# Kernel optimization log

Measured on AMD Instinct MI355X. Metric: run time of the kernel, lower is better.

The kernel has to match this reference:

```python
import jax, jax.numpy as jnp
import numpy as np

B, S, D, H = 4, 2048, 1024, 16
HD = D // H  # head dim = 64


def setup_inputs() -> dict:
    key = jax.random.key(0)
    ks = jax.random.split(key, 6)
    scale = D ** -0.5
    x = jax.random.normal(ks[0], (B, S, D), dtype=jnp.float32)
    # per-head q/k/v projections stacked: [H, D, HD] (bias-free, as in GPT Head)
    Wq = jax.random.normal(ks[1], (H, D, HD), dtype=jnp.float32) * scale
    Wk = jax.random.normal(ks[2], (H, D, HD), dtype=jnp.float32) * scale
    Wv = jax.random.normal(ks[3], (H, D, HD), dtype=jnp.float32) * scale
    # output projection Linear(D, D) with bias
    Wp = jax.random.normal(ks[4], (D, D), dtype=jnp.float32) * scale
    bp = jax.random.normal(ks[5], (D,), dtype=jnp.float32) * 0.01
    return {"x": x, "Wq": Wq, "Wk": Wk, "Wv": Wv, "Wp": Wp, "bp": bp}


def reference(x, Wq, Wk, Wv, Wp, bp):
    # q,k,v: [B, H, S, HD]
    q = jnp.einsum("bsd,hdk->bhsk", x, Wq)
    k = jnp.einsum("bsd,hdk->bhsk", x, Wk)
    v = jnp.einsum("bsd,hdk->bhsk", x, Wv)
    scale = HD ** -0.5
    # attention scores [B, H, S, S] with causal mask
    scores = jnp.einsum("bhsk,bhtk->bhst", q, k) * scale
    causal = jnp.tril(jnp.ones((S, S), dtype=bool))
    scores = jnp.where(causal, scores, jnp.finfo(scores.dtype).min)
    att = jax.nn.softmax(scores, axis=-1)
    out = jnp.einsum("bhst,bhtk->bhsk", att, v)  # [B, H, S, HD]
    # concat heads -> [B, S, D], then output projection
    out = out.transpose(0, 2, 1, 3).reshape(B, S, D)
    return out @ Wp + bp
```

## Files before the change

kernel.cpp:

```cpp
#include <hip/hip_runtime.h>
#include <stdint.h>

#define B_  4
#define S_  2048
#define D_  1024
#define H_  16
#define HD_ 64

typedef __attribute__((ext_vector_type(8))) short bf16x8;
typedef __attribute__((ext_vector_type(4))) short bf16x4;
typedef __attribute__((ext_vector_type(4))) float f32x4;

#define MFMA32(a, b, c) __builtin_amdgcn_mfma_f32_16x16x32_bf16(a, b, c, 0, 0, 0)

__device__ __forceinline__ unsigned short f2bf(float f) {
  union { float f; uint32_t u; } cv; cv.f = f;
  uint32_t x = cv.u;
  uint32_t r = (x + 0x7fffu + ((x >> 16) & 1u)) >> 16;
  return (unsigned short)r;
}

__device__ __forceinline__ unsigned short f2bf_rz(float f) {
  union { float f; uint32_t u; } cv; cv.f = f;
  return (unsigned short)(cv.u >> 16);
}

__device__ __forceinline__ void gload_lds16(const unsigned short* g, unsigned short* l) {
  __builtin_amdgcn_global_load_lds((const __attribute__((address_space(1))) void*)g,
                                   (__attribute__((address_space(3))) void*)l, 16, 0, 0);
}

__global__ void k_cast_x(const float* __restrict__ x, unsigned short* __restrict__ xb) {
  size_t i = ((size_t)blockIdx.x * 256 + threadIdx.x) * 8;
  float4 a = *(const float4*)(x + i);
  float4 b = *(const float4*)(x + i + 4);
  bf16x8 o;
  o[0] = (short)f2bf(a.x); o[1] = (short)f2bf(a.y);
  o[2] = (short)f2bf(a.z); o[3] = (short)f2bf(a.w);
  o[4] = (short)f2bf(b.x); o[5] = (short)f2bf(b.y);
  o[6] = (short)f2bf(b.z); o[7] = (short)f2bf(b.w);
  *(bf16x8*)(xb + i) = o;
}

__global__ void k_wqkv_t(const float* __restrict__ Wq, const float* __restrict__ Wk,
                         const float* __restrict__ Wv, unsigned short* __restrict__ W1T) {
  __shared__ unsigned short tile[64][65];
  const float* W = (blockIdx.z == 0) ? Wq : (blockIdx.z == 1) ? Wk : Wv;
  int h = blockIdx.y;
  int d0 = blockIdx.x * 64;
  int tx = threadIdx.x & 63;
  int tg = threadIdx.x >> 6;
  const float* src = W + (size_t)h * (D_ * HD_) + (size_t)d0 * HD_;
#pragma unroll
  for (int r = 0; r < 16; ++r) {
    int dy = tg * 16 + r;
    tile[tx][dy] = f2bf(src[(size_t)dy * HD_ + tx]);
  }
  __syncthreads();
  unsigned short* dst = W1T + ((size_t)blockIdx.z * 1024 + (size_t)h * 64) * 1024 + d0;
#pragma unroll
  for (int r = 0; r < 16; ++r) {
    int hd = tg * 16 + r;
    dst[(size_t)hd * 1024 + tx] = tile[hd][tx];
  }
}

__global__ void k_wp_t(const float* __restrict__ Wp, unsigned short* __restrict__ WpT) {
  __shared__ unsigned short tile[64][65];
  int n0 = blockIdx.x * 64, k0 = blockIdx.y * 64;
  int tx = threadIdx.x & 63;
  int tg = threadIdx.x >> 6;
#pragma unroll
  for (int r = 0; r < 16; ++r) {
    int ky = tg * 16 + r;
    tile[tx][ky] = f2bf(Wp[(size_t)(k0 + ky) * D_ + n0 + tx]);
  }
  __syncthreads();
#pragma unroll
  for (int r = 0; r < 16; ++r) {
    int ny = tg * 16 + r;
    WpT[(size_t)(n0 + ny) * D_ + k0 + tx] = tile[ny][tx];
  }
}

__device__ __forceinline__ void stage_half(const unsigned short* g0, unsigned short* l0, int tid) {
  int r0 = tid >> 2, s0 = tid & 3;
  gload_lds16(g0 + (size_t)r0 * 1024 + ((s0 ^ ((r0 >> 1) & 3)) << 3), l0 + tid * 8);
  int r1 = r0 + 128;
  gload_lds16(g0 + (size_t)r1 * 1024 + ((s0 ^ ((r1 >> 1) & 3)) << 3), l0 + 4096 + tid * 8);
}

__device__ __forceinline__ bf16x8 rd_swz(const unsigned short* base, int row, int g) {
  return *(const bf16x8*)&base[row * 32 + ((g ^ ((row >> 1) & 3)) << 3)];
}

__global__ __launch_bounds__(512, 2) void k_gemm_qk(const unsigned short* __restrict__ xb,
                                                    const unsigned short* __restrict__ W1T,
                                                    unsigned short* __restrict__ qb,
                                                    unsigned short* __restrict__ kb) {
  __shared__ __align__(16) unsigned short As[32768];
  __shared__ __align__(16) unsigned short Bs[32768];
  int tid = threadIdx.x;
  int lane = tid & 63;
  int wid = tid >> 6;
  int c = lane & 15, g = lane >> 4;
  int wr = wid >> 2, wc = wid & 3;
  int bid = blockIdx.x;
  int xcd = bid & 7, idx = bid >> 3;
  int by = (xcd << 2) | (idx & 3);
  int bx = idx >> 2;
  int m0 = by << 8, n0 = bx << 8;
  const unsigned short* gA = xb + (size_t)m0 * 1024;
  const unsigned short* gB = W1T + (size_t)n0 * 1024;

  f32x4 acc[8][4];
#pragma unroll
  for (int i = 0; i < 8; ++i)
#pragma unroll
    for (int n = 0; n < 4; ++n) acc[i][n] = (f32x4){0.f, 0.f, 0.f, 0.f};

  stage_half(gA + 0,  As + 0, tid);
  stage_half(gB + 0,  Bs + 0, tid);
  stage_half(gA + 32, As + 8192, tid);
  stage_half(gB + 32, Bs + 8192, tid);

  for (int t = 0; t < 16; ++t) {
    int sl = (t & 1) << 14;
    int so = sl ^ 16384;
    int kn = (t + 1) << 6;
    bool pf = (t < 15);
    const unsigned short* Asl = As + sl;
    const unsigned short* Bsl = Bs + sl;
    bf16x8 bf[4];

    asm volatile("s_waitcnt vmcnt(4)" ::: "memory");
    __builtin_amdgcn_s_barrier();
    if (pf) stage_half(gA + kn, As + so, tid);
#pragma unroll
    for (int n = 0; n < 4; ++n) bf[n] = rd_swz(Bsl, wc * 64 + n * 16 + c, g);
    {
      bf16x8 af[4];
#pragma unroll
      for (int j = 0; j < 4; ++j) af[j] = rd_swz(Asl, wr * 128 + j * 16 + c, g);
      __builtin_amdgcn_s_setprio(1);
#pragma unroll
      for (int j = 0; j < 4; ++j)
#pragma unroll
        for (int n = 0; n < 4; ++n) acc[j][n] = MFMA32(af[j], bf[n], acc[j][n]);
      __builtin_amdgcn_s_setprio(0);
    }
    if (pf) stage_half(gB + kn, Bs + so, tid);
    {
      bf16x8 af[4];
#pragma unroll
      for (int j = 0; j < 4; ++j) af[j] = rd_swz(Asl, wr * 128 + (4 + j) * 16 + c, g);
      __builtin_amdgcn_s_setprio(1);
#pragma unroll
      for (int j = 0; j < 4; ++j)
#pragma unroll
        for (int n = 0; n < 4; ++n) acc[4 + j][n] = MFMA32(af[j], bf[n], acc[4 + j][n]);
      __builtin_amdgcn_s_setprio(0);
    }
    asm volatile("s_waitcnt vmcnt(4)" ::: "memory");
    __builtin_amdgcn_s_barrier();
    if (pf) stage_half(gA + kn + 32, As + so + 8192, tid);
#pragma unroll
    for (int n = 0; n < 4; ++n) bf[n] = rd_swz(Bsl + 8192, wc * 64 + n * 16 + c, g);
    {
      bf16x8 af[4];
#pragma unroll
      for (int j = 0; j < 4; ++j) af[j] = rd_swz(Asl + 8192, wr * 128 + j * 16 + c, g);
      __builtin_amdgcn_s_setprio(1);
#pragma unroll
      for (int j = 0; j < 4; ++j)
#pragma unroll
        for (int n = 0; n < 4; ++n) acc[j][n] = MFMA32(af[j], bf[n], acc[j][n]);
      __builtin_amdgcn_s_setprio(0);
    }
    if (pf) stage_half(gB + kn + 32, Bs + so + 8192, tid);
    {
      bf16x8 af[4];
#pragma unroll
      for (int j = 0; j < 4; ++j) af[j] = rd_swz(Asl + 8192, wr * 128 + (4 + j) * 16 + c, g);
      __builtin_amdgcn_s_setprio(1);
#pragma unroll
      for (int j = 0; j < 4; ++j)
#pragma unroll
        for (int n = 0; n < 4; ++n) acc[4 + j][n] = MFMA32(af[j], bf[n], acc[4 + j][n]);
      __builtin_amdgcn_s_setprio(0);
    }
  }

  int Cnb = n0 + wc * 64;
  int qkv = Cnb >> 10;
  int h = (Cnb >> 6) & 15;
  int b = m0 >> 11;
  int s0 = m0 & 2047;
  unsigned short* dst = ((qkv == 0) ? qb : kb) + ((size_t)(b * 16 + h) * S_) * HD_;
  float sc = (qkv == 0) ? 0.125f : 1.0f;
#pragma unroll
  for (int mrep = 0; mrep < 8; ++mrep)
#pragma unroll
    for (int n = 0; n < 4; ++n)
#pragma unroll
      for (int r = 0; r < 4; ++r) {
        int s = s0 + wr * 128 + mrep * 16 + 4 * g + r;
        int hd = n * 16 + c;
        dst[(size_t)s * HD_ + hd] = f2bf(acc[mrep][n][r] * sc);
      }
}

__global__ __launch_bounds__(256) void k_gemm_vt(const unsigned short* __restrict__ W1T,
                                                 const unsigned short* __restrict__ xb,
                                                 unsigned short* __restrict__ vt) {
  __shared__ __align__(16) unsigned short As[128 * 32];
  __shared__ __align__(16) unsigned short Bs[128 * 32];
  const int K = 1024;
  int tid = threadIdx.x;
  int lane = tid & 63;
  int w = tid >> 6;
  int c = lane & 15, g = lane >> 4;
  int wr = w >> 1, wc = w & 1;
  int nwg = gridDim.x * gridDim.y;
  int bid = blockIdx.y * gridDim.x + blockIdx.x;
  int swzb = (bid & 7) * (nwg >> 3) + (bid >> 3);
  int bx = swzb % gridDim.x, by = swzb / gridDim.x;
  int m0 = by * 128;
  int n0 = bx * 128;
  const unsigned short* Av = W1T + (size_t)2048 * 1024;
  f32x4 acc[4][4];
#pragma unroll
  for (int m = 0; m < 4; ++m)
#pragma unroll
    for (int n = 0; n < 4; ++n) acc[m][n] = (f32x4){0.f, 0.f, 0.f, 0.f};

  int t0 = tid, t1 = tid + 256;
  const unsigned short* ga0 = Av + (size_t)(m0 + (t0 >> 2)) * K + 8 * (t0 & 3);
  const unsigned short* ga1 = Av + (size_t)(m0 + (t1 >> 2)) * K + 8 * (t1 & 3);
  const unsigned short* gb0 = xb + (size_t)(n0 + (t0 >> 2)) * K + 8 * (t0 & 3);
  const unsigned short* gb1 = xb + (size_t)(n0 + (t1 >> 2)) * K + 8 * (t1 & 3);

  for (int kk = 0; kk < K; kk += 32) {
    __syncthreads();
    gload_lds16(ga0 + kk, &As[t0 * 8]);
    gload_lds16(ga1 + kk, &As[t1 * 8]);
    gload_lds16(gb0 + kk, &Bs[t0 * 8]);
    gload_lds16(gb1 + kk, &Bs[t1 * 8]);
    __syncthreads();
    bf16x8 af[4], bfr[4];
#pragma unroll
    for (int m = 0; m < 4; ++m)
      af[m] = *(const bf16x8*)&As[(wr * 64 + m * 16 + c) * 32 + 8 * g];
#pragma unroll
    for (int n = 0; n < 4; ++n)
      bfr[n] = *(const bf16x8*)&Bs[(wc * 64 + n * 16 + c) * 32 + 8 * g];
#pragma unroll
    for (int m = 0; m < 4; ++m)
#pragma unroll
      for (int n = 0; n < 4; ++n) acc[m][n] = MFMA32(af[m], bfr[n], acc[m][n]);
  }

  int b = (n0 >> 11);
#pragma unroll
  for (int m = 0; m < 4; ++m)
#pragma unroll
    for (int n = 0; n < 4; ++n)
#pragma unroll
      for (int r = 0; r < 4; ++r) {
        int vm = m0 + wr * 64 + m * 16 + 4 * g + r;
        int Cn = n0 + wc * 64 + n * 16 + c;
        int s = Cn & 2047;
        vt[((size_t)(b << 10) + vm) * S_ + s] = f2bf(acc[m][n][r]);
      }
}

__device__ __forceinline__ void stage_kv(const unsigned short* kp, const unsigned short* vp,
                                         int tb, unsigned short* Ks, unsigned short* Vs,
                                         int tid) {
  int i0 = tid, i1 = tid + 256;
  int r0 = i0 >> 3, ch0 = ((i0 & 7) ^ (r0 & 7)) << 3;
  int r1 = i1 >> 3, ch1 = ((i1 & 7) ^ (r1 & 7)) << 3;
  gload_lds16(kp + (size_t)(tb + r0) * HD_ + ch0, &Ks[i0 * 8]);
  gload_lds16(kp + (size_t)(tb + r1) * HD_ + ch1, &Ks[i1 * 8]);
  gload_lds16(vp + (size_t)r0 * S_ + tb + ch0, &Vs[i0 * 8]);
  gload_lds16(vp + (size_t)r1 * S_ + tb + ch1, &Vs[i1 * 8]);
}

__global__ __launch_bounds__(256) void k_attn(const unsigned short* __restrict__ qb,
                                              const unsigned short* __restrict__ kb,
                                              const unsigned short* __restrict__ vt,
                                              unsigned short* __restrict__ attn) {
  __shared__ __align__(16) unsigned short Ks[2][64 * 64];
  __shared__ __align__(16) unsigned short Vs[2][64 * 64];
  int tid = threadIdx.x;
  int lane = tid & 63;
  int w = tid >> 6;
  int c = lane & 15, g = lane >> 4;
  int swz = ((blockIdx.x & 7) << 6) | (blockIdx.x >> 3);
  int bh = swz >> 3;
  int pr = swz & 7;
  const unsigned short* kp = kb + (size_t)bh * S_ * HD_;
  const unsigned short* vp = vt + (size_t)bh * HD_ * S_;
  int b = bh >> 4, h = bh & 15;

  for (int p = 0; p < 2; ++p) {
    int j = p ? (15 - pr) : pr;
    int q0w = j * 128 + w * 32;
    const unsigned short* qp = qb + ((size_t)bh * S_ + q0w) * HD_;
    bf16x8 qf[2][2];
#pragma unroll
    for (int qs = 0; qs < 2; ++qs)
#pragma unroll
      for (int h2 = 0; h2 < 2; ++h2)
        qf[qs][h2] = *(const bf16x8*)(qp + (size_t)(qs * 16 + c) * HD_ + h2 * 32 + 8 * g);

    const f32x4 fz = {0.f, 0.f, 0.f, 0.f};
    f32x4 oacc[4][2];
#pragma unroll
    for (int c4 = 0; c4 < 4; ++c4)
#pragma unroll
      for (int qs = 0; qs < 2; ++qs) oacc[c4][qs] = fz;
    float m[2] = {-1e30f, -1e30f};
    float l[2] = {0.f, 0.f};

    int nkb = 2 * j + 2;
    int nkw = (q0w + 95) >> 6;

    stage_kv(kp, vp, 0, Ks[0], Vs[0], tid);
    __syncthreads();

    for (int kt = 0; kt < nkb; ++kt) {
      int cur = kt & 1;
      if (kt + 1 < nkb) stage_kv(kp, vp, (kt + 1) << 6, Ks[cur ^ 1], Vs[cur ^ 1], tid);
      if (kt < nkw) {
        int tb = kt << 6;
        const unsigned short* KsC = Ks[cur];
        const unsigned short* VsC = Vs[cur];
        f32x4 st[4][2];
#pragma unroll
        for (int k4 = 0; k4 < 4; ++k4) {
          int row = k4 * 16 + c;
          int rx = row & 7;
          bf16x8 a0 = *(const bf16x8*)&KsC[row * 64 + ((g ^ rx) << 3)];
          bf16x8 a1 = *(const bf16x8*)&KsC[row * 64 + (((4 + g) ^ rx) << 3)];
#pragma unroll
          for (int qs = 0; qs < 2; ++qs) {
            f32x4 t0 = MFMA32(a0, qf[qs][0], fz);
            st[k4][qs] = MFMA32(a1, qf[qs][1], t0);
          }
        }
        if (tb + 63 > q0w) {
#pragma unroll
          for (int k4 = 0; k4 < 4; ++k4)
#pragma unroll
            for (int qs = 0; qs < 2; ++qs)
#pragma unroll
              for (int r = 0; r < 4; ++r)
                if (tb + k4 * 16 + 4 * g + r > q0w + qs * 16 + c) st[k4][qs][r] = -1e30f;
        }
        bf16x8 pa[2][2];
#pragma unroll
        for (int qs = 0; qs < 2; ++qs) {
          float mx = -1e30f;
#pragma unroll
          for (int k4 = 0; k4 < 4; ++k4)
#pragma unroll
            for (int r = 0; r < 4; ++r) mx = fmaxf(mx, st[k4][qs][r]);
          mx = fmaxf(mx, __shfl_xor(mx, 16));
          mx = fmaxf(mx, __shfl_xor(mx, 32));
          if (!__all(mx - m[qs] <= 8.f)) {
            float m_new = fmaxf(m[qs], mx);
            float resc = __expf(m[qs] - m_new);
            m[qs] = m_new;
            float rb0 = __shfl(resc, 4 * g + 0);
            float rb1 = __shfl(resc, 4 * g + 1);
            float rb2 = __shfl(resc, 4 * g + 2);
            float rb3 = __shfl(resc, 4 * g + 3);
#pragma unroll
            for (int c4 = 0; c4 < 4; ++c4) {
              oacc[c4][qs][0] *= rb0; oacc[c4][qs][1] *= rb1;
              oacc[c4][qs][2] *= rb2; oacc[c4][qs][3] *= rb3;
            }
            l[qs] *= resc;
          }
          float mh = m[qs];
          float rs = 0.f;
#pragma unroll
          for (int k4 = 0; k4 < 4; ++k4)
#pragma unroll
            for (int r = 0; r < 4; ++r) {
              float e = __expf(st[k4][qs][r] - mh);
              st[k4][qs][r] = e;
              rs += e;
            }
          rs += __shfl_xor(rs, 16);
          rs += __shfl_xor(rs, 32);
          l[qs] += rs;
#pragma unroll
          for (int ks = 0; ks < 2; ++ks)
#pragma unroll
            for (int jj = 0; jj < 8; ++jj)
              pa[qs][ks][jj] = (short)f2bf_rz(st[ks * 2 + (jj >> 2)][qs][jj & 3]);
        }
#pragma unroll
        for (int c4 = 0; c4 < 4; ++c4) {
          int row = c4 * 16 + c;
          int rx = row & 7;
#pragma unroll
          for (int ks = 0; ks < 2; ++ks) {
            int e0 = ks * 32 + 4 * g;
            int e1 = e0 + 16;
            int s0 = (((e0 >> 3) ^ rx) << 3) | (e0 & 7);
            int s1 = (((e1 >> 3) ^ rx) << 3) | (e1 & 7);
            bf16x4 v0 = *(const bf16x4*)&VsC[row * 64 + s0];
            bf16x4 v1 = *(const bf16x4*)&VsC[row * 64 + s1];
            bf16x8 vf;
            vf[0] = v0[0]; vf[1] = v0[1]; vf[2] = v0[2]; vf[3] = v0[3];
            vf[4] = v1[0]; vf[5] = v1[1]; vf[6] = v1[2]; vf[7] = v1[3];
#pragma unroll
            for (int qs = 0; qs < 2; ++qs)
              oacc[c4][qs] = MFMA32(pa[qs][ks], vf, oacc[c4][qs]);
          }
        }
      }
      __syncthreads();
    }
#pragma unroll
    for (int qs = 0; qs < 2; ++qs) {
      float linv = 1.f / l[qs];
      float lb0 = __shfl(linv, 4 * g + 0);
      float lb1 = __shfl(linv, 4 * g + 1);
      float lb2 = __shfl(linv, 4 * g + 2);
      float lb3 = __shfl(linv, 4 * g + 3);
      float lb[4] = {lb0, lb1, lb2, lb3};
      unsigned short* op = attn + ((size_t)b * S_ + q0w + qs * 16) * D_ + h * HD_;
#pragma unroll
      for (int c4 = 0; c4 < 4; ++c4)
#pragma unroll
        for (int r = 0; r < 4; ++r)
          op[(size_t)(4 * g + r) * D_ + c4 * 16 + c] = f2bf(oacc[c4][qs][r] * lb[r]);
    }
  }
}

__global__ __launch_bounds__(256) void k_gemm_out(const unsigned short* __restrict__ at,
                                                  const unsigned short* __restrict__ WpT,
                                                  const float* __restrict__ bp,
                                                  float* __restrict__ out) {
  __shared__ __align__(16) unsigned short As[128 * 32];
  __shared__ __align__(16) unsigned short Bs[128 * 32];
  const int K = 1024;
  int tid = threadIdx.x;
  int lane = tid & 63;
  int w = tid >> 6;
  int c = lane & 15, g = lane >> 4;
  int wr = w >> 1, wc = w & 1;
  int nwg = gridDim.x * gridDim.y;
  int bid = blockIdx.y * gridDim.x + blockIdx.x;
  int swzb = (bid & 7) * (nwg >> 3) + (bid >> 3);
  int bx = swzb % gridDim.x, by = swzb / gridDim.x;
  int m0 = by * 128;
  int n0 = bx * 128;
  f32x4 acc[4][4];
#pragma unroll
  for (int m = 0; m < 4; ++m)
#pragma unroll
    for (int n = 0; n < 4; ++n) acc[m][n] = (f32x4){0.f, 0.f, 0.f, 0.f};

  int t0 = tid, t1 = tid + 256;
  const unsigned short* ga0 = at + (size_t)(m0 + (t0 >> 2)) * K + 8 * (t0 & 3);
  const unsigned short* ga1 = at + (size_t)(m0 + (t1 >> 2)) * K + 8 * (t1 & 3);
  const unsigned short* gb0 = WpT + (size_t)(n0 + (t0 >> 2)) * K + 8 * (t0 & 3);
  const unsigned short* gb1 = WpT + (size_t)(n0 + (t1 >> 2)) * K + 8 * (t1 & 3);

  for (int kk = 0; kk < K; kk += 32) {
    __syncthreads();
    gload_lds16(ga0 + kk, &As[t0 * 8]);
    gload_lds16(ga1 + kk, &As[t1 * 8]);
    gload_lds16(gb0 + kk, &Bs[t0 * 8]);
    gload_lds16(gb1 + kk, &Bs[t1 * 8]);
    __syncthreads();
    bf16x8 af[4], bfr[4];
#pragma unroll
    for (int m = 0; m < 4; ++m)
      af[m] = *(const bf16x8*)&As[(wr * 64 + m * 16 + c) * 32 + 8 * g];
#pragma unroll
    for (int n = 0; n < 4; ++n)
      bfr[n] = *(const bf16x8*)&Bs[(wc * 64 + n * 16 + c) * 32 + 8 * g];
#pragma unroll
    for (int m = 0; m < 4; ++m)
#pragma unroll
      for (int n = 0; n < 4; ++n) acc[m][n] = MFMA32(af[m], bfr[n], acc[m][n]);
  }

#pragma unroll
  for (int m = 0; m < 4; ++m)
#pragma unroll
    for (int n = 0; n < 4; ++n)
#pragma unroll
      for (int r = 0; r < 4; ++r) {
        int R = m0 + wr * 64 + m * 16 + 4 * g + r;
        int Cn = n0 + wc * 64 + n * 16 + c;
        out[(size_t)R * D_ + Cn] = acc[m][n][r] + bp[Cn];
      }
}

extern "C" void kernel_launch(void* const* d_in, const int* in_sizes, int n_in,
                              void* d_out, int out_size, void* d_ws, size_t ws_size,
                              hipStream_t stream) {
  const float* x  = (const float*)d_in[0];
  const float* Wq = (const float*)d_in[1];
  const float* Wk = (const float*)d_in[2];
  const float* Wv = (const float*)d_in[3];
  const float* Wp = (const float*)d_in[4];
  const float* bp = (const float*)d_in[5];
  float* out = (float*)d_out;
  char* ws = (char*)d_ws;
  unsigned short* xb  = (unsigned short*)(ws);
  unsigned short* w1t = (unsigned short*)(ws + (size_t)(16u << 20));
  unsigned short* wpt = (unsigned short*)(ws + (size_t)(22u << 20));
  unsigned short* qb  = (unsigned short*)(ws + (size_t)(24u << 20));
  unsigned short* kb  = (unsigned short*)(ws + (size_t)(40u << 20));
  unsigned short* vt  = (unsigned short*)(ws + (size_t)(56u << 20));
  unsigned short* at  = xb;

  k_cast_x<<<dim3(4096), dim3(256), 0, stream>>>(x, xb);
  k_wqkv_t<<<dim3(16, 16, 3), dim3(256), 0, stream>>>(Wq, Wk, Wv, w1t);
  k_wp_t<<<dim3(16, 16), dim3(256), 0, stream>>>(Wp, wpt);
  k_gemm_qk<<<dim3(256), dim3(512), 0, stream>>>(xb, w1t, qb, kb);
  k_gemm_vt<<<dim3(64, 8), dim3(256), 0, stream>>>(w1t, xb, vt);
  k_attn<<<dim3(512), dim3(256), 0, stream>>>(qb, kb, vt, at);
  k_gemm_out<<<dim3(8, 64), dim3(256), 0, stream>>>(at, wpt, bp, out);
}
```

Before: 184.8 us.

## Halve attention query tile per block, double grid, use exp2 with folded log2e scale

```diff
diff --git a/kernel.cpp b/kernel.cpp
--- a/kernel.cpp
+++ b/kernel.cpp
@@ -23,6 +23,14 @@
 __device__ __forceinline__ unsigned short f2bf_rz(float f) {
   union { float f; uint32_t u; } cv; cv.f = f;
   return (unsigned short)(cv.u >> 16);
+}
+
+__device__ __forceinline__ float fexp2(float x) {
+#if __has_builtin(__builtin_amdgcn_exp2f)
+  return __builtin_amdgcn_exp2f(x);
+#else
+  return exp2f(x);
+#endif
 }
 
 __device__ __forceinline__ void gload_lds16(const unsigned short* g, unsigned short* l) {
@@ -197,7 +205,7 @@
   int b = m0 >> 11;
   int s0 = m0 & 2047;
   unsigned short* dst = ((qkv == 0) ? qb : kb) + ((size_t)(b * 16 + h) * S_) * HD_;
-  float sc = (qkv == 0) ? 0.125f : 1.0f;
+  float sc = (qkv == 0) ? 0.18033688011112042f : 1.0f;
 #pragma unroll
   for (int mrep = 0; mrep < 8; ++mrep)
 #pragma unroll
@@ -296,35 +304,29 @@
   int lane = tid & 63;
   int w = tid >> 6;
   int c = lane & 15, g = lane >> 4;
-  int swz = ((blockIdx.x & 7) << 6) | (blockIdx.x >> 3);
-  int bh = swz >> 3;
-  int pr = swz & 7;
+  int swz = ((blockIdx.x & 7) << 7) | (blockIdx.x >> 3);
+  int bh = swz >> 4;
+  int pr = swz & 15;
   const unsigned short* kp = kb + (size_t)bh * S_ * HD_;
   const unsigned short* vp = vt + (size_t)bh * HD_ * S_;
   int b = bh >> 4, h = bh & 15;
 
   for (int p = 0; p < 2; ++p) {
-    int j = p ? (15 - pr) : pr;
-    int q0w = j * 128 + w * 32;
+    int j = p ? (31 - pr) : pr;
+    int q0w = j * 64 + w * 16;
     const unsigned short* qp = qb + ((size_t)bh * S_ + q0w) * HD_;
-    bf16x8 qf[2][2];
-#pragma unroll
-    for (int qs = 0; qs < 2; ++qs)
-#pragma unroll
-      for (int h2 = 0; h2 < 2; ++h2)
-        qf[qs][h2] = *(const bf16x8*)(qp + (size_t)(qs * 16 + c) * HD_ + h2 * 32 + 8 * g);
+    bf16x8 qf[2];
+#pragma unroll
+    for (int h2 = 0; h2 < 2; ++h2)
+      qf[h2] = *(const bf16x8*)(qp + (size_t)c * HD_ + h2 * 32 + 8 * g);
 
     const f32x4 fz = {0.f, 0.f, 0.f, 0.f};
-    f32x4 oacc[4][2];
-#pragma unroll
-    for (int c4 = 0; c4 < 4; ++c4)
-#pragma unroll
-      for (int qs = 0; qs < 2; ++qs) oacc[c4][qs] = fz;
-    float m[2] = {-1e30f, -1e30f};
-    float l[2] = {0.f, 0.f};
-
-    int nkb = 2 * j + 2;
-    int nkw = (q0w + 95) >> 6;
+    f32x4 oacc[4];
+#pragma unroll
+    for (int c4 = 0; c4 < 4; ++c4) oacc[c4] = fz;
+    float m = -1e30f, l = 0.f;
+
+    int nkb = j + 1;
 
     stage_kv(kp, vp, 0, Ks[0], Vs[0], tid);
     __syncthreads();
@@ -332,76 +334,67 @@
     for (int kt = 0; kt < nkb; ++kt) {
       int cur = kt & 1;
       if (kt + 1 < nkb) stage_kv(kp, vp, (kt + 1) << 6, Ks[cur ^ 1], Vs[cur ^ 1], tid);
-      if (kt < nkw) {
+      {
         int tb = kt << 6;
         const unsigned short* KsC = Ks[cur];
         const unsigned short* VsC = Vs[cur];
-        f32x4 st[4][2];
+        f32x4 st[4];
 #pragma unroll
         for (int k4 = 0; k4 < 4; ++k4) {
           int row = k4 * 16 + c;
           int rx = row & 7;
           bf16x8 a0 = *(const bf16x8*)&KsC[row * 64 + ((g ^ rx) << 3)];
           bf16x8 a1 = *(const bf16x8*)&KsC[row * 64 + (((4 + g) ^ rx) << 3)];
-#pragma unroll
-          for (int qs = 0; qs < 2; ++qs) {
-            f32x4 t0 = MFMA32(a0, qf[qs][0], fz);
-            st[k4][qs] = MFMA32(a1, qf[qs][1], t0);
-          }
+          f32x4 t0 = MFMA32(a0, qf[0], fz);
+          st[k4] = MFMA32(a1, qf[1], t0);
         }
         if (tb + 63 > q0w) {
 #pragma unroll
           for (int k4 = 0; k4 < 4; ++k4)
 #pragma unroll
-            for (int qs = 0; qs < 2; ++qs)
-#pragma unroll
-              for (int r = 0; r < 4; ++r)
-                if (tb + k4 * 16 + 4 * g + r > q0w + qs * 16 + c) st[k4][qs][r] = -1e30f;
+            for (int r = 0; r < 4; ++r)
+              if (tb + k4 * 16 + 4 * g + r > q0w + c) st[k4][r] = -1e30f;
         }
-        bf16x8 pa[2][2];
-#pragma unroll
-        for (int qs = 0; qs < 2; ++qs) {
-          float mx = -1e30f;
-#pragma unroll
-          for (int k4 = 0; k4 < 4; ++k4)
-#pragma unroll
-            for (int r = 0; r < 4; ++r) mx = fmaxf(mx, st[k4][qs][r]);
-          mx = fmaxf(mx, __shfl_xor(mx, 16));
-          mx = fmaxf(mx, __shfl_xor(mx, 32));
-          if (!__all(mx - m[qs] <= 8.f)) {
-            float m_new = fmaxf(m[qs], mx);
-            float resc = __expf(m[qs] - m_new);
-            m[qs] = m_new;
-            float rb0 = __shfl(resc, 4 * g + 0);
-            float rb1 = __shfl(resc, 4 * g + 1);
-            float rb2 = __shfl(resc, 4 * g + 2);
-            float rb3 = __shfl(resc, 4 * g + 3);
-#pragma unroll
-            for (int c4 = 0; c4 < 4; ++c4) {
-              oacc[c4][qs][0] *= rb0; oacc[c4][qs][1] *= rb1;
-              oacc[c4][qs][2] *= rb2; oacc[c4][qs][3] *= rb3;
-            }
-            l[qs] *= resc;
+        float mx = -1e30f;
+#pragma unroll
+        for (int k4 = 0; k4 < 4; ++k4)
+#pragma unroll
+          for (int r = 0; r < 4; ++r) mx = fmaxf(mx, st[k4][r]);
+        mx = fmaxf(mx, __shfl_xor(mx, 16));
+        mx = fmaxf(mx, __shfl_xor(mx, 32));
+        if (!__all(mx - m <= 8.f)) {
+          float m_new = fmaxf(m, mx);
+          float resc = fexp2(m - m_new);
+          m = m_new;
+          float rb0 = __shfl(resc, 4 * g + 0);
+          float rb1 = __shfl(resc, 4 * g + 1);
+          float rb2 = __shfl(resc, 4 * g + 2);
+          float rb3 = __shfl(resc, 4 * g + 3);
+#pragma unroll
+          for (int c4 = 0; c4 < 4; ++c4) {
+            oacc[c4][0] *= rb0; oacc[c4][1] *= rb1;
+            oacc[c4][2] *= rb2; oacc[c4][3] *= rb3;
           }
-          float mh = m[qs];
-          float rs = 0.f;
-#pragma unroll
-          for (int k4 = 0; k4 < 4; ++k4)
-#pragma unroll
-            for (int r = 0; r < 4; ++r) {
-              float e = __expf(st[k4][qs][r] - mh);
-              st[k4][qs][r] = e;
-              rs += e;
-            }
-          rs += __shfl_xor(rs, 16);
-          rs += __shfl_xor(rs, 32);
-          l[qs] += rs;
-#pragma unroll
-          for (int ks = 0; ks < 2; ++ks)
-#pragma unroll
-            for (int jj = 0; jj < 8; ++jj)
-              pa[qs][ks][jj] = (short)f2bf_rz(st[ks * 2 + (jj >> 2)][qs][jj & 3]);
+          l *= resc;
         }
+        float rs = 0.f;
+#pragma unroll
+        for (int k4 = 0; k4 < 4; ++k4)
+#pragma unroll
+          for (int r = 0; r < 4; ++r) {
+            float e = fexp2(st[k4][r] - m);
+            st[k4][r] = e;
+            rs += e;
+          }
+        rs += __shfl_xor(rs, 16);
+        rs += __shfl_xor(rs, 32);
+        l += rs;
+        bf16x8 pa[2];
+#pragma unroll
+        for (int ks = 0; ks < 2; ++ks)
+#pragma unroll
+          for (int jj = 0; jj < 8; ++jj)
+            pa[ks][jj] = (short)f2bf_rz(st[ks * 2 + (jj >> 2)][jj & 3]);
 #pragma unroll
         for (int c4 = 0; c4 < 4; ++c4) {
           int row = c4 * 16 + c;
@@ -417,29 +410,24 @@
             bf16x8 vf;
             vf[0] = v0[0]; vf[1] = v0[1]; vf[2] = v0[2]; vf[3] = v0[3];
             vf[4] = v1[0]; vf[5] = v1[1]; vf[6] = v1[2]; vf[7] = v1[3];
-#pragma unroll
-            for (int qs = 0; qs < 2; ++qs)
-              oacc[c4][qs] = MFMA32(pa[qs][ks], vf, oacc[c4][qs]);
+            oacc[c4] = MFMA32(pa[ks], vf, oacc[c4]);
           }
         }
       }
       __syncthreads();
     }
-#pragma unroll
-    for (int qs = 0; qs < 2; ++qs) {
-      float linv = 1.f / l[qs];
-      float lb0 = __shfl(linv, 4 * g + 0);
-      float lb1 = __shfl(linv, 4 * g + 1);
-      float lb2 = __shfl(linv, 4 * g + 2);
-      float lb3 = __shfl(linv, 4 * g + 3);
-      float lb[4] = {lb0, lb1, lb2, lb3};
-      unsigned short* op = attn + ((size_t)b * S_ + q0w + qs * 16) * D_ + h * HD_;
-#pragma unroll
-      for (int c4 = 0; c4 < 4; ++c4)
-#pragma unroll
-        for (int r = 0; r < 4; ++r)
-          op[(size_t)(4 * g + r) * D_ + c4 * 16 + c] = f2bf(oacc[c4][qs][r] * lb[r]);
-    }
+    float linv = 1.f / l;
+    float lb0 = __shfl(linv, 4 * g + 0);
+    float lb1 = __shfl(linv, 4 * g + 1);
+    float lb2 = __shfl(linv, 4 * g + 2);
+    float lb3 = __shfl(linv, 4 * g + 3);
+    float lb[4] = {lb0, lb1, lb2, lb3};
+    unsigned short* op = attn + ((size_t)b * S_ + q0w) * D_ + h * HD_;
+#pragma unroll
+    for (int c4 = 0; c4 < 4; ++c4)
+#pragma unroll
+      for (int r = 0; r < 4; ++r)
+        op[(size_t)(4 * g + r) * D_ + c4 * 16 + c] = f2bf(oacc[c4][r] * lb[r]);
   }
 }
 
@@ -529,6 +517,6 @@
   k_wp_t<<<dim3(16, 16), dim3(256), 0, stream>>>(Wp, wpt);
   k_gemm_qk<<<dim3(256), dim3(512), 0, stream>>>(xb, w1t, qb, kb);
   k_gemm_vt<<<dim3(64, 8), dim3(256), 0, stream>>>(w1t, xb, vt);
-  k_attn<<<dim3(512), dim3(256), 0, stream>>>(qb, kb, vt, at);
+  k_attn<<<dim3(1024), dim3(256), 0, stream>>>(qb, kb, vt, at);
   k_gemm_out<<<dim3(8, 64), dim3(256), 0, stream>>>(at, wpt, bp, out);
 }
```

Result: slower. 200.0 us (+8.2%).
